# Kernel optimization log

Hardware: AMD Instinct MI355X
Metric: run time of the kernel (lower is better)

Reference implementation:

```python
import jax, jax.numpy as jnp
import numpy as np

B, IN_SEQ, HID_SEQ, OUT_SEQ = 2, 2048, 2048, 2048
C_IN, C_OUT, H = 1024, 1024, 16
HD = C_OUT // H  # 64


def _linear_params(key, out_f, in_f):
    kw, kb = jax.random.split(key)
    bound = 1.0 / np.sqrt(in_f)
    w = jax.random.uniform(kw, (out_f, in_f), jnp.float32, -bound, bound)
    b = jax.random.uniform(kb, (out_f,), jnp.float32, -bound, bound)
    return w, b


def setup_inputs() -> dict:
    key = jax.random.key(0)
    ks = jax.random.split(key, 6)
    x = jax.random.normal(ks[0], (B, IN_SEQ, C_IN), jnp.float32)
    w_hseq, b_hseq = _linear_params(ks[1], HID_SEQ, IN_SEQ)
    wq, bq = _linear_params(ks[2], C_OUT, C_IN)
    wk, bk = _linear_params(ks[3], C_OUT, C_IN)
    wv, bv = _linear_params(ks[4], C_OUT, C_IN)
    w_oseq, b_oseq = _linear_params(ks[5], OUT_SEQ, HID_SEQ)
    return {"x": x, "w_hseq": w_hseq, "b_hseq": b_hseq,
            "wq": wq, "bq": bq, "wk": wk, "bk": bk, "wv": wv, "bv": bv,
            "w_oseq": w_oseq, "b_oseq": b_oseq}


def reference(x, w_hseq, b_hseq, wq, bq, wk, bk, wv, bv, w_oseq, b_oseq):
    b = x.shape[0]
    # seq-axis projection: Linear(in_seq -> hidden_seq) applied to x.transpose(1,2)
    # xh[b, t, c] = sum_s x[b, s, c] * w_hseq[t, s] + b_hseq[t]
    xh = jnp.einsum('bsc,ts->btc', x, w_hseq) + b_hseq[:, None]
    q = (xh @ wq.T + bq).reshape(b, HID_SEQ, H, HD).transpose(0, 2, 1, 3)  # [B,H,Sh,hd]
    k = (xh @ wk.T + bk).reshape(b, HID_SEQ, H, HD).transpose(0, 2, 1, 3)
    v = (xh @ wv.T + bv).reshape(b, HID_SEQ, H, HD).transpose(0, 2, 1, 3)
    scores = jnp.einsum('bhqd,bhkd->bhqk', q, k) / np.sqrt(HD).astype(np.float32)
    attn = jax.nn.softmax(scores, axis=-1)                       # [B,H,Sh,Sh]
    flex = jnp.einsum('bhqk,ok->bhqo', attn, w_oseq) + b_oseq    # [B,H,Sh,So]
    # flexscale.transpose(-2,-1) @ v contracts over the QUERY axis q
    out = jnp.einsum('bhqo,bhqd->bhod', flex, v)                 # [B,H,So,hd]
    return out.transpose(0, 2, 1, 3).reshape(b, OUT_SEQ, C_OUT)
```

## Files before the change

### kernel.cpp

```cpp
#include <hip/hip_runtime.h>
#include <hip/hip_bf16.h>

typedef unsigned short u16;
typedef unsigned int u32;
typedef unsigned long long u64;
typedef __attribute__((ext_vector_type(8))) short s16x8;
typedef __attribute__((ext_vector_type(4))) u32 u32x4;
typedef __attribute__((ext_vector_type(4))) float f32x4;
typedef __attribute__((ext_vector_type(16))) float f32x16;

#define SCL 0.1803368867f

#if __has_builtin(__builtin_amdgcn_exp2f)
#define EXP2(x) __builtin_amdgcn_exp2f(x)
#else
#define EXP2(x) exp2f(x)
#endif

__device__ __forceinline__ float bf2f(u16 v){ u32 u = ((u32)v)<<16; return __builtin_bit_cast(float,u); }
__device__ __forceinline__ u16 f2bf(float f){
  u32 u = __builtin_bit_cast(u32,f);
  u += 0x7fff + ((u>>16)&1);
  return (u16)(u>>16);
}
__device__ __forceinline__ u32 pkbf(float a, float b){
  u32 ua = __builtin_bit_cast(u32,a) + 0x8000u;
  u32 ub = __builtin_bit_cast(u32,b) + 0x8000u;
  return (ua>>16) | (ub & 0xFFFF0000u);
}
__device__ __forceinline__ void glds16(const u16* g, const u16* lds_u){
  __builtin_amdgcn_global_load_lds(
      (const __attribute__((address_space(1))) void*)(u64)g,
      (__attribute__((address_space(3))) void*)(u32)(u64)lds_u,
      16, 0, 0);
}
__device__ __forceinline__ f32x4 mfma16(s16x8 a, s16x8 b, f32x4 c){
  return __builtin_amdgcn_mfma_f32_16x16x32_bf16(a,b,c,0,0,0);
}
__device__ __forceinline__ f32x16 mfma32(s16x8 a, s16x8 b, f32x16 c){
  return __builtin_amdgcn_mfma_f32_32x32x16_bf16(a,b,c,0,0,0);
}

__global__ __launch_bounds__(256) void detect_dtype(const u16* __restrict__ x, u32* __restrict__ flag){
  __shared__ int cnt;
  if (threadIdx.x==0) cnt = 0;
  __syncthreads();
  int local = 0;
  for (int i = threadIdx.x; i < 4096; i += 256){
    u16 v = x[2*i];
    int e = (v>>7)&0xFF;
    if (e >= 140 || e <= 100) local++;
  }
  atomicAdd(&cnt, local);
  __syncthreads();
  if (threadIdx.x==0) *flag = (cnt > 1024) ? 1u : 0u;
}

struct CvtArgs { const void* src[10]; u16* dst[10]; int n[10]; };

__global__ __launch_bounds__(256) void convert_all(
    CvtArgs a, const void* __restrict__ xsrc,
    const u32* __restrict__ flag, u16* __restrict__ xT)
{
  __shared__ u16 T[64][72];
  const int t = threadIdx.x;
  if (blockIdx.y < 10){
    const int which = blockIdx.y;
    const int n = a.n[which];
    const int base = blockIdx.x*2048 + t;
    if (base >= n) return;
    u16* dst = a.dst[which];
    if (*flag){
      const float* s = (const float*)a.src[which];
      #pragma unroll
      for (int j=0;j<8;j++){ int i = base + j*256; if (i<n) dst[i] = f2bf(s[i]); }
    } else {
      const u16* s = (const u16*)a.src[which];
      #pragma unroll
      for (int j=0;j<8;j++){ int i = base + j*256; if (i<n) dst[i] = s[i]; }
    }
    return;
  }
  const int bx = blockIdx.x;
  if (bx >= 1024) return;
  const int s0 = (bx&31)*64, c0 = ((bx>>5)&15)*64, b = bx>>9;
  const int r = t>>2, cc = (t&3)*16;
  const long off = ((long)(b*2048 + s0 + r))*1024 + c0 + cc;
  if (*flag){
    const float* p = (const float*)xsrc + off;
    #pragma unroll
    for (int j=0;j<16;j++) T[r][cc+j] = f2bf(p[j]);
  } else {
    const u16* p = (const u16*)xsrc + off;
    *(s16x8*)&T[r][cc]   = *(const s16x8*)p;
    *(s16x8*)&T[r][cc+8] = *(const s16x8*)(p+8);
  }
  __syncthreads();
  {
    const int orow = t&63, oc = (t>>6)*16;
    u16 tmp[16];
    #pragma unroll
    for (int j=0;j<16;j++) tmp[j] = T[oc+j][orow];
    u16* q = xT + (long)b*2097152 + (long)(c0+orow)*2048 + s0 + oc;
    *(s16x8*)q     = *(s16x8*)&tmp[0];
    *(s16x8*)(q+8) = *(s16x8*)&tmp[8];
  }
}

__global__ __launch_bounds__(256) void rowsum_mt(const u16* __restrict__ Mt, float* __restrict__ sv){
  const int row = blockIdx.x*4 + (threadIdx.x>>6);
  const int lane = threadIdx.x&63;
  const u16* p = Mt + (long)row*2048;
  float s = 0.f;
  #pragma unroll
  for (int i=0;i<4;i++){
    s16x8 v = *(const s16x8*)&p[i*512 + lane*8];
    #pragma unroll
    for (int j=0;j<8;j++) s += bf2f((u16)v[j]);
  }
  #pragma unroll
  for (int off=32; off>=1; off>>=1) s += __shfl_xor(s, off);
  if (lane==0) sv[row] = s;
}

template<int BN, int BMODE, bool DYN, bool QS>
__global__ __launch_bounds__(256) void gemm_t(
    const u16* __restrict__ A, const u16* __restrict__ B,
    const u16* __restrict__ bias, const float* __restrict__ r1col,
    const u32* __restrict__ dflag, void* __restrict__ C,
    int K, int lda, int ldb, int ldc,
    long aBatch, long bBatch, long cBatch)
{
  constexpr int BM = 128;
  constexpr int ACH = BM/64, BCH = BN/64;
  constexpr int MI = (BN==128) ? 4 : 2;
  __shared__ u16 As[2][BM*32];
  __shared__ u16 Bs[2][BN*32];
  const int t = threadIdx.x, w = t>>6, quad = (t&63)>>4, l16 = t&15;
  const int z = blockIdx.z;
  const int m0 = blockIdx.x*BM, n0 = blockIdx.y*BN;
  const u16* Ag = A + (long)z*aBatch + (long)m0*lda;
  const u16* Bg = B + (long)z*bBatch + (long)n0*ldb;
  const int wm = (BN==128) ? (w>>1)*64 : w*32;
  const int wn = (BN==128) ? (w&1)*64 : 0;

  auto stage = [&](int buf, int k0){
    #pragma unroll
    for (int i=0;i<ACH;i++){
      const int chunk = i*256 + t;
      glds16(Ag + (long)(chunk>>2)*lda + k0 + (chunk&3)*8, &As[buf][(i*256 + w*64)*8]);
    }
    #pragma unroll
    for (int i=0;i<BCH;i++){
      const int chunk = i*256 + t;
      glds16(Bg + (long)(chunk>>2)*ldb + k0 + (chunk&3)*8, &Bs[buf][(i*256 + w*64)*8]);
    }
  };

  f32x4 acc[MI][4];
  #pragma unroll
  for (int i=0;i<MI;i++)
    #pragma unroll
    for (int j=0;j<4;j++) acc[i][j] = (f32x4){0.f,0.f,0.f,0.f};

  stage(0, 0);
  const int nk = K>>5;
  for (int kt=0; kt<nk; ++kt){
    __syncthreads();
    if (kt+1 < nk) stage((kt+1)&1, (kt+1)<<5);
    const u16* as = As[kt&1];
    const u16* bs = Bs[kt&1];
    s16x8 a[MI], bb[4];
    #pragma unroll
    for (int i=0;i<MI;i++) a[i] = *(const s16x8*)&as[(wm + i*16 + l16)*32 + quad*8];
    #pragma unroll
    for (int j=0;j<4;j++)  bb[j]= *(const s16x8*)&bs[(wn + j*16 + l16)*32 + quad*8];
    #pragma unroll
    for (int i=0;i<MI;i++)
      #pragma unroll
      for (int j=0;j<4;j++)
        acc[i][j] = mfma16(a[i], bb[j], acc[i][j]);
  }

  bool f32o = false;
  if (DYN) f32o = (*dflag != 0);
  #pragma unroll
  for (int i=0;i<MI;i++){
    #pragma unroll
    for (int j=0;j<4;j++){
      const int col = n0 + wn + j*16 + l16;
      #pragma unroll
      for (int r=0;r<4;r++){
        const int row = m0 + wm + i*16 + quad*4 + r;
        float vv = acc[i][j][r];
        if (BMODE==1) vv += bf2f(bias[row]);
        if (BMODE==2) vv += bf2f(bias[col]);
        if (BMODE==3) vv += bf2f(bias[row]) * r1col[z*1024 + col];
        if (QS){ if (col < 1024) vv *= SCL; }
        const long idx = (long)z*cBatch + (long)row*ldc + col;
        if (DYN && f32o) ((float*)C)[idx] = vv;
        else             ((u16*)C)[idx]   = f2bf(vv);
      }
    }
  }
}

__global__ __launch_bounds__(256) void attn_stats(const u16* __restrict__ qkv, u16* __restrict__ VtG){
  __shared__ u16 Qs[64][68];
  __shared__ u16 Ks[2][64][68];
  __shared__ float red[2][64];
  __shared__ float ilv[64];
  const int q0 = blockIdx.x*64, bh = blockIdx.y, b = bh>>4, h = bh&15;
  const int t = threadIdx.x, w = t>>6, l32 = t&31, half = (t&63)>>5;
  const int wq = w>>1, wk = w&1;
  const int r = t>>2, cc = (t&3)*16;
  {
    const u16* p = &qkv[((long)(b*2048 + q0 + r))*3072 + h*64 + cc];
    *(s16x8*)&Qs[r][cc]   = *(const s16x8*)p;
    *(s16x8*)&Qs[r][cc+8] = *(const s16x8*)(p+8);
  }
  const u16* kg = &qkv[((long)(b*2048 + r))*3072 + 1024 + h*64 + cc];
  s16x8 sk0 = *(const s16x8*)kg;
  s16x8 sk1 = *(const s16x8*)(kg+8);
  *(s16x8*)&Ks[0][r][cc]   = sk0;
  *(s16x8*)&Ks[0][r][cc+8] = sk1;
  sk0 = *(const s16x8*)(kg + (long)64*3072);
  sk1 = *(const s16x8*)(kg + (long)64*3072 + 8);
  __syncthreads();
  s16x8 aq[4];
  #pragma unroll
  for (int u=0;u<4;u++) aq[u] = *(s16x8*)&Qs[wq*32 + l32][u*16 + half*8];
  float lp[16];
  #pragma unroll
  for (int r2=0;r2<16;r2++) lp[r2] = 0.f;

  for (int kc=0; kc<32; ++kc){
    __syncthreads();
    const int cur = kc&1;
    if (kc+1 < 32){
      *(s16x8*)&Ks[cur^1][r][cc]   = sk0;
      *(s16x8*)&Ks[cur^1][r][cc+8] = sk1;
      if (kc+2 < 32){
        sk0 = *(const s16x8*)(kg + (long)(kc+2)*64*3072);
        sk1 = *(const s16x8*)(kg + (long)(kc+2)*64*3072 + 8);
      }
    }
    s16x8 kb[4];
    #pragma unroll
    for (int u=0;u<4;u++) kb[u] = *(s16x8*)&Ks[cur][wk*32 + l32][u*16 + half*8];
    f32x16 acc = {};
    #pragma unroll
    for (int u=0;u<4;u++) acc = mfma32(aq[u], kb[u], acc);
    #pragma unroll
    for (int r2=0;r2<16;r2++) lp[r2] += EXP2(acc[r2]);
  }
  #pragma unroll
  for (int off=1; off<32; off<<=1)
    #pragma unroll
    for (int r2=0;r2<16;r2++) lp[r2] += __shfl_xor(lp[r2], off);
  if (l32 == 0){
    #pragma unroll
    for (int r2=0;r2<16;r2++)
      red[wk][wq*32 + 4*half + (r2&3) + 8*(r2>>2)] = lp[r2];
  }
  __syncthreads();
  if (t < 64) ilv[t] = 1.f / (red[0][t] + red[1][t]);
  __syncthreads();
  {
    const u16* p = &qkv[((long)(b*2048 + q0 + r))*3072 + 2048 + h*64 + cc];
    const float sc = ilv[r];
    s16x8 v0 = *(const s16x8*)p, v1 = *(const s16x8*)(p+8);
    #pragma unroll
    for (int j=0;j<8;j++){
      Qs[r][cc+j]   = f2bf(bf2f((u16)v0[j])*sc);
      Qs[r][cc+8+j] = f2bf(bf2f((u16)v1[j])*sc);
    }
  }
  __syncthreads();
  {
    const int orow = t&63, oc = (t>>6)*16;
    u16 tmp[16];
    #pragma unroll
    for (int j=0;j<16;j++) tmp[j] = Qs[oc+j][orow];
    u16* q = VtG + (long)b*2097152 + (long)(h*64+orow)*2048 + q0 + oc;
    *(s16x8*)q     = *(s16x8*)&tmp[0];
    *(s16x8*)(q+8) = *(s16x8*)&tmp[8];
  }
}

__global__ __launch_bounds__(256,2) void attn_pv(
    const u16* __restrict__ qkv, const u16* __restrict__ VtG, u16* __restrict__ Mt)
{
  __shared__ u16 Qs[2][64][68];
  __shared__ u16 Vs[2][64][68];
  const int t = threadIdx.x, w = t>>6, l32 = t&31, hi = (t&63)>>5;
  const int bh = blockIdx.y, b = bh>>4, h = bh&15;
  const int kcol = blockIdx.x*128 + w*32 + l32;
  const int r = t>>2, cc = (t&3)*16;

  const u16* kp = qkv + ((long)(b*2048 + kcol))*3072 + 1024 + h*64 + hi*8;
  s16x8 kb[4];
  #pragma unroll
  for (int c=0;c<4;c++) kb[c] = *(const s16x8*)(kp + c*16);

  const u16* qg = &qkv[((long)(b*2048 + r))*3072 + h*64 + cc];
  const u16* vg = &VtG[((long)(b*1024 + h*64 + r))*2048 + cc];

  s16x8 sq0 = *(const s16x8*)qg, sq1 = *(const s16x8*)(qg+8);
  s16x8 sv0 = *(const s16x8*)vg, sv1 = *(const s16x8*)(vg+8);
  *(s16x8*)&Qs[0][r][cc]   = sq0;  *(s16x8*)&Qs[0][r][cc+8] = sq1;
  *(s16x8*)&Vs[0][r][cc]   = sv0;  *(s16x8*)&Vs[0][r][cc+8] = sv1;
  {
    const u16* nq = qg + (long)64*3072;
    const u16* nv = vg + 64;
    sq0 = *(const s16x8*)nq; sq1 = *(const s16x8*)(nq+8);
    sv0 = *(const s16x8*)nv; sv1 = *(const s16x8*)(nv+8);
  }

  f32x16 accM0 = {}, accM1 = {};
  for (int i=0; i<32; ++i){
    __syncthreads();
    const int cur = i&1;
    if (i+1 < 32){
      *(s16x8*)&Qs[cur^1][r][cc]   = sq0;  *(s16x8*)&Qs[cur^1][r][cc+8] = sq1;
      *(s16x8*)&Vs[cur^1][r][cc]   = sv0;  *(s16x8*)&Vs[cur^1][r][cc+8] = sv1;
      if (i+2 < 32){
        const u16* nq = qg + (long)(i+2)*64*3072;
        const u16* nv = vg + (i+2)*64;
        sq0 = *(const s16x8*)nq; sq1 = *(const s16x8*)(nq+8);
        sv0 = *(const s16x8*)nv; sv1 = *(const s16x8*)(nv+8);
      }
    }
    s16x8 aq0[4], aq1[4];
    #pragma unroll
    for (int c=0;c<4;c++){
      aq0[c] = *(s16x8*)&Qs[cur][l32][c*16 + hi*8];
      aq1[c] = *(s16x8*)&Qs[cur][32+l32][c*16 + hi*8];
    }
    f32x16 acc0 = {}, acc1 = {};
    #pragma unroll
    for (int c=0;c<4;c++){
      acc0 = mfma32(aq0[c], kb[c], acc0);
      acc1 = mfma32(aq1[c], kb[c], acc1);
    }
    s16x8 bp[4];
    #pragma unroll
    for (int qt=0;qt<2;qt++){
      float p[16];
      #pragma unroll
      for (int r2=0;r2<16;r2++) p[r2] = EXP2(qt ? acc1[r2] : acc0[r2]);
      #pragma unroll
      for (int ccc=0; ccc<2; ccc++){
        u32 X0, X1, Y0, Y1;
        asm("v_cvt_pk_bf16_f32 %0, %1, %2" : "=v"(X0) : "v"(p[ccc*8+0]), "v"(p[ccc*8+1]));
        asm("v_cvt_pk_bf16_f32 %0, %1, %2" : "=v"(X1) : "v"(p[ccc*8+2]), "v"(p[ccc*8+3]));
        asm("v_cvt_pk_bf16_f32 %0, %1, %2" : "=v"(Y0) : "v"(p[ccc*8+4]), "v"(p[ccc*8+5]));
        asm("v_cvt_pk_bf16_f32 %0, %1, %2" : "=v"(Y1) : "v"(p[ccc*8+6]), "v"(p[ccc*8+7]));
        asm volatile("v_permlane32_swap_b32 %0, %1" : "+v"(X0), "+v"(Y0));
        asm volatile("v_permlane32_swap_b32 %0, %1" : "+v"(X1), "+v"(Y1));
        u32x4 dw; dw[0]=X0; dw[1]=X1; dw[2]=Y0; dw[3]=Y1;
        bp[qt*2+ccc] = __builtin_bit_cast(s16x8, dw);
      }
    }
    s16x8 av0[4], av1[4];
    #pragma unroll
    for (int c=0;c<4;c++){
      av0[c] = *(s16x8*)&Vs[cur][l32][c*16 + hi*8];
      av1[c] = *(s16x8*)&Vs[cur][32+l32][c*16 + hi*8];
    }
    #pragma unroll
    for (int c=0;c<4;c++){
      accM0 = mfma32(av0[c], bp[c], accM0);
      accM1 = mfma32(av1[c], bp[c], accM1);
    }
  }
  #pragma unroll
  for (int r2=0;r2<16;r2++){
    const int d0 = 4*hi + (r2&3) + 8*(r2>>2);
    Mt[((long)(b*1024 + h*64 + d0))*2048 + kcol]      = f2bf(accM0[r2]);
    Mt[((long)(b*1024 + h*64 + d0 + 32))*2048 + kcol] = f2bf(accM1[r2]);
  }
}

extern "C" void kernel_launch(void* const* d_in, const int* in_sizes, int n_in,
                              void* d_out, int out_size, void* d_ws, size_t ws_size,
                              hipStream_t stream)
{
  (void)n_in; (void)out_size; (void)ws_size;
  char* ws = (char*)d_ws;
  u32*  dflag = (u32*)ws;            ws += 64;
  u16*  whc   = (u16*)ws;            ws += (size_t)8388608;
  u16*  wqkvc = (u16*)ws;            ws += (size_t)6291456;
  u16*  woc   = (u16*)ws;            ws += (size_t)8388608;
  u16*  bhc   = (u16*)ws;            ws += 4096;
  u16*  bqkvc = (u16*)ws;            ws += 8192;
  u16*  boc   = (u16*)ws;            ws += 4096;
  u16*  xT    = (u16*)ws;            ws += (size_t)8388608;
  u16*  xh    = (u16*)ws;            ws += (size_t)8388608;
  u16*  qkvb  = (u16*)ws;            ws += (size_t)25165824;
  u16*  VtG   = (u16*)ws;            ws += (size_t)8388608;
  u16*  Mt    = (u16*)ws;            ws += (size_t)8388608;
  float* sv   = (float*)ws;          ws += 8192;

  detect_dtype<<<1,256,0,stream>>>((const u16*)d_in[0], dflag);
  CvtArgs ca;
  const void* srcs[10] = {d_in[1], d_in[2], d_in[3], d_in[4], d_in[5],
                          d_in[6], d_in[7], d_in[8], d_in[9], d_in[10]};
  u16* dsts[10] = {whc, bhc, wqkvc, bqkvc, wqkvc+1048576, bqkvc+1024,
                   wqkvc+2097152, bqkvc+2048, woc, boc};
  const int ns[10] = {in_sizes[1], in_sizes[2], in_sizes[3], in_sizes[4], in_sizes[5],
                      in_sizes[6], in_sizes[7], in_sizes[8], in_sizes[9], in_sizes[10]};
  for (int i=0;i<10;i++){ ca.src[i]=srcs[i]; ca.dst[i]=dsts[i]; ca.n[i]=ns[i]; }
  convert_all<<<dim3(2048,11),256,0,stream>>>(ca, d_in[0], dflag, xT);

  const long S2M = 2097152L;

  gemm_t<64,1,false,false><<<dim3(16,16,2),256,0,stream>>>(whc, xT, bhc, nullptr, dflag, xh,
      2048, 2048, 2048, 1024, 0L, S2M, S2M);

  gemm_t<128,2,false,true><<<dim3(16,24,2),256,0,stream>>>(xh, wqkvc, bqkvc, nullptr, dflag, qkvb,
      1024, 1024, 1024, 3072, S2M, 0L, (long)2048*3072);

  attn_stats<<<dim3(32,32),256,0,stream>>>(qkvb, VtG);

  attn_pv<<<dim3(16,32),256,0,stream>>>(qkvb, VtG, Mt);

  rowsum_mt<<<512,256,0,stream>>>(Mt, sv);

  gemm_t<64,3,true,false><<<dim3(16,16,2),256,0,stream>>>(woc, Mt, boc, sv, dflag, d_out,
      2048, 2048, 2048, 1024, 0L, S2M, S2M);
}
```

Before: 310.4 us.

## Widen attn_pv blocks to 512 threads and raise priority around MFMA bursts

Each attn_pv block now has 8 waves and covers 256 key columns instead of 128, so each staged Q/V tile in shared memory is reused by twice as many waves. The grid is halved, and each thread loads one 16-byte chunk per tile instead of two. s_setprio is raised around the MFMA sequences in attn_stats and attn_pv so matrix work gets issue priority over other waves. The risks are fewer blocks (256) to fill the CUs, more waves stalling at each barrier, and register pressure under the 512-thread launch bound.

New measurement: 294.3 us. 5.2% less time.

```diff
diff --git a/kernel.cpp b/kernel.cpp
--- a/kernel.cpp
+++ b/kernel.cpp
@@ -249,8 +249,10 @@
     #pragma unroll
     for (int u=0;u<4;u++) kb[u] = *(s16x8*)&Ks[cur][wk*32 + l32][u*16 + half*8];
     f32x16 acc = {};
+    __builtin_amdgcn_s_setprio(1);
     #pragma unroll
     for (int u=0;u<4;u++) acc = mfma32(aq[u], kb[u], acc);
+    __builtin_amdgcn_s_setprio(0);
     #pragma unroll
     for (int r2=0;r2<16;r2++) lp[r2] += EXP2(acc[r2]);
   }
@@ -288,15 +290,15 @@
   }
 }
 
-__global__ __launch_bounds__(256,2) void attn_pv(
+__global__ __launch_bounds__(512,2) void attn_pv(
     const u16* __restrict__ qkv, const u16* __restrict__ VtG, u16* __restrict__ Mt)
 {
   __shared__ u16 Qs[2][64][68];
   __shared__ u16 Vs[2][64][68];
   const int t = threadIdx.x, w = t>>6, l32 = t&31, hi = (t&63)>>5;
   const int bh = blockIdx.y, b = bh>>4, h = bh&15;
-  const int kcol = blockIdx.x*128 + w*32 + l32;
-  const int r = t>>2, cc = (t&3)*16;
+  const int kcol = blockIdx.x*256 + w*32 + l32;
+  const int r = t>>3, cc = (t&7)*8;
 
   const u16* kp = qkv + ((long)(b*2048 + kcol))*3072 + 1024 + h*64 + hi*8;
   s16x8 kb[4];
@@ -306,29 +308,23 @@
   const u16* qg = &qkv[((long)(b*2048 + r))*3072 + h*64 + cc];
   const u16* vg = &VtG[((long)(b*1024 + h*64 + r))*2048 + cc];
 
-  s16x8 sq0 = *(const s16x8*)qg, sq1 = *(const s16x8*)(qg+8);
-  s16x8 sv0 = *(const s16x8*)vg, sv1 = *(const s16x8*)(vg+8);
-  *(s16x8*)&Qs[0][r][cc]   = sq0;  *(s16x8*)&Qs[0][r][cc+8] = sq1;
-  *(s16x8*)&Vs[0][r][cc]   = sv0;  *(s16x8*)&Vs[0][r][cc+8] = sv1;
-  {
-    const u16* nq = qg + (long)64*3072;
-    const u16* nv = vg + 64;
-    sq0 = *(const s16x8*)nq; sq1 = *(const s16x8*)(nq+8);
-    sv0 = *(const s16x8*)nv; sv1 = *(const s16x8*)(nv+8);
-  }
+  s16x8 sq = *(const s16x8*)qg;
+  s16x8 sv = *(const s16x8*)vg;
+  *(s16x8*)&Qs[0][r][cc] = sq;
+  *(s16x8*)&Vs[0][r][cc] = sv;
+  sq = *(const s16x8*)(qg + (long)64*3072);
+  sv = *(const s16x8*)(vg + 64);
 
   f32x16 accM0 = {}, accM1 = {};
   for (int i=0; i<32; ++i){
     __syncthreads();
     const int cur = i&1;
     if (i+1 < 32){
-      *(s16x8*)&Qs[cur^1][r][cc]   = sq0;  *(s16x8*)&Qs[cur^1][r][cc+8] = sq1;
-      *(s16x8*)&Vs[cur^1][r][cc]   = sv0;  *(s16x8*)&Vs[cur^1][r][cc+8] = sv1;
+      *(s16x8*)&Qs[cur^1][r][cc] = sq;
+      *(s16x8*)&Vs[cur^1][r][cc] = sv;
       if (i+2 < 32){
-        const u16* nq = qg + (long)(i+2)*64*3072;
-        const u16* nv = vg + (i+2)*64;
-        sq0 = *(const s16x8*)nq; sq1 = *(const s16x8*)(nq+8);
-        sv0 = *(const s16x8*)nv; sv1 = *(const s16x8*)(nv+8);
+        sq = *(const s16x8*)(qg + (long)(i+2)*64*3072);
+        sv = *(const s16x8*)(vg + (i+2)*64);
       }
     }
     s16x8 aq0[4], aq1[4];
@@ -338,11 +334,13 @@
       aq1[c] = *(s16x8*)&Qs[cur][32+l32][c*16 + hi*8];
     }
     f32x16 acc0 = {}, acc1 = {};
+    __builtin_amdgcn_s_setprio(1);
     #pragma unroll
     for (int c=0;c<4;c++){
       acc0 = mfma32(aq0[c], kb[c], acc0);
       acc1 = mfma32(aq1[c], kb[c], acc1);
     }
+    __builtin_amdgcn_s_setprio(0);
     s16x8 bp[4];
     #pragma unroll
     for (int qt=0;qt<2;qt++){
@@ -368,11 +366,13 @@
       av0[c] = *(s16x8*)&Vs[cur][l32][c*16 + hi*8];
       av1[c] = *(s16x8*)&Vs[cur][32+l32][c*16 + hi*8];
     }
+    __builtin_amdgcn_s_setprio(1);
     #pragma unroll
     for (int c=0;c<4;c++){
       accM0 = mfma32(av0[c], bp[c], accM0);
       accM1 = mfma32(av1[c], bp[c], accM1);
     }
+    __builtin_amdgcn_s_setprio(0);
   }
   #pragma unroll
   for (int r2=0;r2<16;r2++){
@@ -423,7 +423,7 @@
 
   attn_stats<<<dim3(32,32),256,0,stream>>>(qkvb, VtG);
 
-  attn_pv<<<dim3(16,32),256,0,stream>>>(qkvb, VtG, Mt);
+  attn_pv<<<dim3(8,32),512,0,stream>>>(qkvb, VtG, Mt);
 
   rowsum_mt<<<512,256,0,stream>>>(Mt, sv);
 
```

## Split attn_pv over query halves and combine fp32 partials in rowsum kernel

Applied to the files above, without the earlier changes.

The attn_pv grid gains a z dimension that splits the query-axis reduction into two halves. This doubles the number of blocks (512 to 1024) to improve occupancy across CUs, and each block runs 16 iterations instead of 32. Each half writes fp32 partial sums to separate buffers, which are aliased onto weight and activation workspace that is dead by then. The rowsum kernel becomes combine_mt, which adds the partials, rounds to bf16, writes Mt and computes the row sums. It costs extra fp32 write/read traffic. attn_stats also gains s_setprio around its MFMA block.

Result: no change. 307.6 us (-0.9%).

```diff
diff --git a/kernel.cpp b/kernel.cpp
--- a/kernel.cpp
+++ b/kernel.cpp
@@ -22,11 +22,6 @@
   u32 u = __builtin_bit_cast(u32,f);
   u += 0x7fff + ((u>>16)&1);
   return (u16)(u>>16);
-}
-__device__ __forceinline__ u32 pkbf(float a, float b){
-  u32 ua = __builtin_bit_cast(u32,a) + 0x8000u;
-  u32 ub = __builtin_bit_cast(u32,b) + 0x8000u;
-  return (ua>>16) | (ub & 0xFFFF0000u);
 }
 __device__ __forceinline__ void glds16(const u16* g, const u16* lds_u){
   __builtin_amdgcn_global_load_lds(
@@ -107,16 +102,29 @@
   }
 }
 
-__global__ __launch_bounds__(256) void rowsum_mt(const u16* __restrict__ Mt, float* __restrict__ sv){
+__global__ __launch_bounds__(256) void combine_mt(
+    const float* __restrict__ F0, const float* __restrict__ F1,
+    u16* __restrict__ Mt, float* __restrict__ sv)
+{
   const int row = blockIdx.x*4 + (threadIdx.x>>6);
   const int lane = threadIdx.x&63;
-  const u16* p = Mt + (long)row*2048;
+  const float* p0 = F0 + (long)row*2048;
+  const float* p1 = F1 + (long)row*2048;
+  u16* q = Mt + (long)row*2048;
   float s = 0.f;
   #pragma unroll
-  for (int i=0;i<4;i++){
-    s16x8 v = *(const s16x8*)&p[i*512 + lane*8];
-    #pragma unroll
-    for (int j=0;j<8;j++) s += bf2f((u16)v[j]);
+  for (int i=0;i<8;i++){
+    const int o = i*256 + lane*4;
+    f32x4 a = *(const f32x4*)&p0[o];
+    f32x4 c = *(const f32x4*)&p1[o];
+    u64 pk = 0;
+    #pragma unroll
+    for (int j=0;j<4;j++){
+      u16 bv = f2bf(a[j]+c[j]);
+      s += bf2f(bv);
+      pk |= ((u64)bv) << (16*j);
+    }
+    *(u64*)&q[o] = pk;
   }
   #pragma unroll
   for (int off=32; off>=1; off>>=1) s += __shfl_xor(s, off);
@@ -249,8 +257,10 @@
     #pragma unroll
     for (int u=0;u<4;u++) kb[u] = *(s16x8*)&Ks[cur][wk*32 + l32][u*16 + half*8];
     f32x16 acc = {};
+    __builtin_amdgcn_s_setprio(1);
     #pragma unroll
     for (int u=0;u<4;u++) acc = mfma32(aq[u], kb[u], acc);
+    __builtin_amdgcn_s_setprio(0);
     #pragma unroll
     for (int r2=0;r2<16;r2++) lp[r2] += EXP2(acc[r2]);
   }
@@ -289,12 +299,14 @@
 }
 
 __global__ __launch_bounds__(256,2) void attn_pv(
-    const u16* __restrict__ qkv, const u16* __restrict__ VtG, u16* __restrict__ Mt)
+    const u16* __restrict__ qkv, const u16* __restrict__ VtG,
+    float* __restrict__ F0, float* __restrict__ F1)
 {
   __shared__ u16 Qs[2][64][68];
   __shared__ u16 Vs[2][64][68];
   const int t = threadIdx.x, w = t>>6, l32 = t&31, hi = (t&63)>>5;
   const int bh = blockIdx.y, b = bh>>4, h = bh&15;
+  const int qh = blockIdx.z;
   const int kcol = blockIdx.x*128 + w*32 + l32;
   const int r = t>>2, cc = (t&3)*16;
 
@@ -303,8 +315,8 @@
   #pragma unroll
   for (int c=0;c<4;c++) kb[c] = *(const s16x8*)(kp + c*16);
 
-  const u16* qg = &qkv[((long)(b*2048 + r))*3072 + h*64 + cc];
-  const u16* vg = &VtG[((long)(b*1024 + h*64 + r))*2048 + cc];
+  const u16* qg = &qkv[((long)(b*2048 + qh*1024 + r))*3072 + h*64 + cc];
+  const u16* vg = &VtG[((long)(b*1024 + h*64 + r))*2048 + qh*1024 + cc];
 
   s16x8 sq0 = *(const s16x8*)qg, sq1 = *(const s16x8*)(qg+8);
   s16x8 sv0 = *(const s16x8*)vg, sv1 = *(const s16x8*)(vg+8);
@@ -318,13 +330,13 @@
   }
 
   f32x16 accM0 = {}, accM1 = {};
-  for (int i=0; i<32; ++i){
+  for (int i=0; i<16; ++i){
     __syncthreads();
     const int cur = i&1;
-    if (i+1 < 32){
+    if (i+1 < 16){
       *(s16x8*)&Qs[cur^1][r][cc]   = sq0;  *(s16x8*)&Qs[cur^1][r][cc+8] = sq1;
       *(s16x8*)&Vs[cur^1][r][cc]   = sv0;  *(s16x8*)&Vs[cur^1][r][cc+8] = sv1;
-      if (i+2 < 32){
+      if (i+2 < 16){
         const u16* nq = qg + (long)(i+2)*64*3072;
         const u16* nv = vg + (i+2)*64;
         sq0 = *(const s16x8*)nq; sq1 = *(const s16x8*)(nq+8);
@@ -374,11 +386,12 @@
       accM1 = mfma32(av1[c], bp[c], accM1);
     }
   }
+  float* out = qh ? F1 : F0;
   #pragma unroll
   for (int r2=0;r2<16;r2++){
     const int d0 = 4*hi + (r2&3) + 8*(r2>>2);
-    Mt[((long)(b*1024 + h*64 + d0))*2048 + kcol]      = f2bf(accM0[r2]);
-    Mt[((long)(b*1024 + h*64 + d0 + 32))*2048 + kcol] = f2bf(accM1[r2]);
+    out[((long)(b*1024 + h*64 + d0))*2048 + kcol]      = accM0[r2];
+    out[((long)(b*1024 + h*64 + d0 + 32))*2048 + kcol] = accM1[r2];
   }
 }
 
@@ -389,14 +402,16 @@
   (void)n_in; (void)out_size; (void)ws_size;
   char* ws = (char*)d_ws;
   u32*  dflag = (u32*)ws;            ws += 64;
-  u16*  whc   = (u16*)ws;            ws += (size_t)8388608;
-  u16*  wqkvc = (u16*)ws;            ws += (size_t)6291456;
+  u16*  whc   = (u16*)ws;
+  float* MtF0 = (float*)ws;          ws += (size_t)16777216;
+  u16*  wqkvc = whc + 4194304;
+  u16*  xT    = (u16*)ws;
+  float* MtF1 = (float*)ws;          ws += (size_t)16777216;
+  u16*  xh    = xT + 4194304;
   u16*  woc   = (u16*)ws;            ws += (size_t)8388608;
   u16*  bhc   = (u16*)ws;            ws += 4096;
   u16*  bqkvc = (u16*)ws;            ws += 8192;
   u16*  boc   = (u16*)ws;            ws += 4096;
-  u16*  xT    = (u16*)ws;            ws += (size_t)8388608;
-  u16*  xh    = (u16*)ws;            ws += (size_t)8388608;
   u16*  qkvb  = (u16*)ws;            ws += (size_t)25165824;
   u16*  VtG   = (u16*)ws;            ws += (size_t)8388608;
   u16*  Mt    = (u16*)ws;            ws += (size_t)8388608;
@@ -423,9 +438,9 @@
 
   attn_stats<<<dim3(32,32),256,0,stream>>>(qkvb, VtG);
 
-  attn_pv<<<dim3(16,32),256,0,stream>>>(qkvb, VtG, Mt);
-
-  rowsum_mt<<<512,256,0,stream>>>(Mt, sv);
+  attn_pv<<<dim3(16,32,2),256,0,stream>>>(qkvb, VtG, MtF0, MtF1);
+
+  combine_mt<<<512,256,0,stream>>>(MtF0, MtF1, Mt, sv);
 
   gemm_t<64,3,true,false><<<dim3(16,16,2),256,0,stream>>>(woc, Mt, boc, sv, dflag, d_out,
       2048, 2048, 2048, 1024, 0L, S2M, S2M);
```
